# Kernel optimization log

Hardware: AMD Instinct MI355X
Metric: run time of the kernel (lower is better)

Reference implementation:

```python
import jax, jax.numpy as jnp
import numpy as np

# dims chosen per input_specs / init_kwargs
B, S, D_IN, UNITS, WIN = 4, 2048, 512, 64, 32
W = 2 * WIN + 1  # max window length


def setup_inputs() -> dict:
    key = jax.random.key(0)
    ks = jax.random.split(key, 8)
    p = lambda k, shape: jax.random.normal(k, shape, dtype=jnp.float32) * 0.02
    return {
        "query": jax.random.normal(ks[0], (B, S, D_IN), dtype=jnp.float32),
        "value": jax.random.normal(ks[1], (B, S, D_IN), dtype=jnp.float32),
        "Wq": p(ks[2], (D_IN, UNITS)), "bq": jnp.zeros((UNITS,), jnp.float32),
        "Wk": p(ks[3], (D_IN, UNITS)), "bk": jnp.zeros((UNITS,), jnp.float32),
        "Wv": p(ks[4], (D_IN, UNITS)), "bv": jnp.zeros((UNITS,), jnp.float32),
    }


def reference(query, value, Wq, bq, Wk, bk, Wv, bv):
    # Dense projections (query stream -> Q, value stream -> K and V)
    Q = query @ Wq + bq
    K = value @ Wk + bk
    V = value @ Wv + bv

    i = np.arange(S)
    start = np.maximum(i - WIN, 0)            # [S]
    end = np.minimum(i + WIN + 1, S)          # [S]
    lengths = end - start                      # [S] window length per position
    offsets = np.concatenate([[0], np.cumsum(lengths)[:-1]])
    L = int(lengths.sum())                     # total output seq length (concat of all windows)

    idx = start[:, None] + np.arange(W)[None, :]   # [S, W] window token indices
    valid = idx < end[:, None]                      # [S, W] which slots exist
    idx_c = np.minimum(idx, S - 1)                  # clamp for safe gather

    idx_c = jnp.asarray(idx_c)
    valid_j = jnp.asarray(valid)

    # Gather overlapping windows: [B, S, W, UNITS]
    Ql = Q[:, idx_c]
    Kl = K[:, idx_c]
    Vl = V[:, idx_c]

    # Faithful to original: ALL window rows act as queries for window i.
    scale = 1.0 / jnp.sqrt(jnp.asarray(UNITS, dtype=Q.dtype))
    scores = jnp.einsum("bswd,bsud->bswu", Ql, Kl) * scale  # [B, S, W, W]
    neg = jnp.finfo(scores.dtype).min
    scores = jnp.where(valid_j[None, :, None, :], scores, neg)  # mask padded keys
    weights = jax.nn.softmax(scores, axis=-1)
    out_local = jnp.einsum("bswu,bsud->bswd", weights, Vl)  # [B, S, W, UNITS]

    # Concat valid rows of every window along seq axis -> [B, L, UNITS]
    flat_pos = jnp.asarray(offsets)[:, None] + jnp.arange(W)[None, :]  # [S, W]
    flat_pos = jnp.where(valid_j, flat_pos, L)  # invalid rows dumped in slot L
    out = jnp.zeros((Q.shape[0], L + 1, UNITS), dtype=out_local.dtype)
    out = out.at[:, flat_pos.reshape(-1)].set(out_local.reshape(Q.shape[0], -1, UNITS))
    return out[:, :L]
```

## Files before the change

kernel.cpp:

```cpp
#include <hip/hip_runtime.h>
#include <hip/hip_bf16.h>

#define BB 4
#define SS 2048
#define DIN 512
#define UU 64
#define WINR 32
#define LTOT 132064
#define GQ 16
#define VST 200

typedef __attribute__((ext_vector_type(8))) short short8;
typedef __attribute__((ext_vector_type(4))) float float4v;
typedef __attribute__((ext_vector_type(4))) uint uint4v;

static __device__ __forceinline__ ushort f2bf(float f) {
    union { __hip_bfloat16 h; ushort u; } c;
    c.h = __float2bfloat16(f);
    return c.u;
}
static __device__ __forceinline__ float bf2f(ushort u) {
    union { float f; uint v; } c;
    c.v = ((uint)u) << 16;
    return c.f;
}
static __device__ __forceinline__ float bfbits(uint u) {
    union { float f; uint v; } c;
    c.v = u;
    return c.f;
}

__device__ __forceinline__ int offs_of(int s) {
    int a = s < (SS - 33) ? s : (SS - 33);
    int m = (s - 33) > 0 ? (s - 33) : 0;
    return a * (a - 1) / 2 + 33 * a + (s - a) * SS - m * (m + 1) / 2;
}

__global__ __launch_bounds__(256) void prep_w(
    const float* __restrict__ Wq, const float* __restrict__ Wk, const float* __restrict__ Wv,
    ushort* __restrict__ Wt)
{
    __shared__ float T[64][65];
    const int mtx = blockIdx.x >> 3;
    const int kc  = blockIdx.x & 7;
    const float* W = (mtx == 0) ? Wq : ((mtx == 1) ? Wk : Wv);
    const int tid = threadIdx.x;
    for (int idx = tid; idx < 64 * 64; idx += 256) {
        const int k = idx >> 6, n = idx & 63;
        T[n][k] = W[(size_t)(kc * 64 + k) * UU + n];
    }
    __syncthreads();
    for (int idx = tid; idx < 64 * 64; idx += 256) {
        const int n = idx >> 6, kl = idx & 63;
        Wt[(size_t)mtx * UU * DIN + (size_t)n * DIN + kc * 64 + kl] = f2bf(T[n][kl]);
    }
}

__global__ __launch_bounds__(256) void qkv_mfma(
    const float* __restrict__ query, const float* __restrict__ value,
    const ushort* __restrict__ Wt,
    const float* __restrict__ bq, const float* __restrict__ bk, const float* __restrict__ bv,
    float* __restrict__ Qs, ushort* __restrict__ Kf, ushort* __restrict__ Vf)
{
    __shared__ float red[4][16 * UU];
    const int bid = blockIdx.x;
    const int mtx = bid >> 9;
    const int rt  = bid & 511;
    const int tid = threadIdx.x;
    const int kq = tid >> 6;
    const int lane = tid & 63;
    const int m16 = lane & 15, quad = lane >> 4;

    const float* X = (mtx == 0) ? query : value;
    const float* Xrow = X + (size_t)(rt * 16 + m16) * DIN + kq * 128 + quad * 8;
    const ushort* Wm = Wt + (size_t)mtx * UU * DIN + (size_t)m16 * DIN + kq * 128 + quad * 8;

    float4v acc[4];
#pragma unroll
    for (int nb = 0; nb < 4; ++nb) acc[nb] = (float4v){0.f, 0.f, 0.f, 0.f};

#pragma unroll
    for (int kk = 0; kk < 4; ++kk) {
        const float4 xa = *(const float4*)(Xrow + kk * 32);
        const float4 xb = *(const float4*)(Xrow + kk * 32 + 4);
        short8 a;
        a[0] = (short)f2bf(xa.x); a[1] = (short)f2bf(xa.y);
        a[2] = (short)f2bf(xa.z); a[3] = (short)f2bf(xa.w);
        a[4] = (short)f2bf(xb.x); a[5] = (short)f2bf(xb.y);
        a[6] = (short)f2bf(xb.z); a[7] = (short)f2bf(xb.w);
#pragma unroll
        for (int nb = 0; nb < 4; ++nb) {
            const short8 bfr = *(const short8*)(Wm + (size_t)nb * 16 * DIN + kk * 32);
            acc[nb] = __builtin_amdgcn_mfma_f32_16x16x32_bf16(a, bfr, acc[nb], 0, 0, 0);
        }
    }

#pragma unroll
    for (int nb = 0; nb < 4; ++nb)
#pragma unroll
        for (int reg = 0; reg < 4; ++reg)
            red[kq][(quad * 4 + reg) * UU + nb * 16 + m16] = acc[nb][reg];
    __syncthreads();

    const float* bias = (mtx == 0) ? bq : ((mtx == 1) ? bk : bv);
#pragma unroll
    for (int i = 0; i < 4; ++i) {
        const int e = tid + 256 * i;
        const int col = e & 63, row = e >> 6;
        float s = red[0][e] + red[1][e] + red[2][e] + red[3][e] + bias[col];
        const size_t gi = (size_t)(rt * 16 + row) * UU + col;
        if (mtx == 0)      Qs[gi] = s * 0.125f;
        else if (mtx == 1) Kf[gi] = f2bf(s);
        else               Vf[gi] = f2bf(s);
    }
}

__global__ __launch_bounds__(1024, 8) void attn_kernel(
    const float* __restrict__ Qs, const ushort* __restrict__ Kf,
    const ushort* __restrict__ Vf, float* __restrict__ out)
{
    __shared__ __align__(16) ushort Vt[UU * VST];
    __shared__ __align__(16) float  evf[GQ * VST];

    const int blk = blockIdx.x;
    const int b = blk >> 7;
    const int q0 = (blk & 127) << 4;
    const int tid = threadIdx.x;
    const int lane = tid & 63;
    const int wq = __builtin_amdgcn_readfirstlane(tid >> 6);

    const int j0 = max(q0 - 2 * WINR, 0);
    const int j1 = min(q0 + GQ - 1 + 2 * WINR + 1, SS);
    const int nw = j1 - j0;

    {
        const uint4v z = (uint4v){0u, 0u, 0u, 0u};
        uint4v* V4 = (uint4v*)Vt;
        uint4v* E4 = (uint4v*)evf;
        for (int i = tid; i < 1600; i += 1024) V4[i] = z;
        for (int i = tid; i < 800;  i += 1024) E4[i] = z;
    }
    __syncthreads();

    if (wq >= 9) {
        const uint* Vg = (const uint*)(Vf + ((size_t)b * SS + j0) * UU);
        for (int idx = tid - 9 * 64; idx < nw * 32; idx += 7 * 64) {
            const int j = idx >> 5, d2 = idx & 31;
            const uint v = Vg[idx];
            Vt[(2 * d2) * VST + 40 + j]     = (ushort)v;
            Vt[(2 * d2 + 1) * VST + 40 + j] = (ushort)(v >> 16);
        }
    } else {
        const int t = wq;
        const int m16 = lane & 15, quad = lane >> 4;
        const int jb = j0 + 16 * t + m16;
        const int jr = jb < SS ? jb : SS - 1;
        const ushort* kr = Kf + ((size_t)b * SS + jr) * UU + quad * 8;
        const float*  qr = Qs + ((size_t)b * SS + q0 + m16) * UU + quad * 8;
        const short8 kb0 = *(const short8*)(kr);
        const short8 kb1 = *(const short8*)(kr + 32);
        short8 ah0, al0, ah1, al1;
#pragma unroll
        for (int e = 0; e < 8; ++e) {
            const float qa = qr[e], qb = qr[e + 32];
            const ushort h0 = f2bf(qa);
            ah0[e] = (short)h0; al0[e] = (short)f2bf(qa - bf2f(h0));
            const ushort h1 = f2bf(qb);
            ah1[e] = (short)h1; al1[e] = (short)f2bf(qb - bf2f(h1));
        }
        float4v acc = (float4v){0.f, 0.f, 0.f, 0.f};
        acc = __builtin_amdgcn_mfma_f32_16x16x32_bf16(ah0, kb0, acc, 0, 0, 0);
        acc = __builtin_amdgcn_mfma_f32_16x16x32_bf16(al0, kb0, acc, 0, 0, 0);
        acc = __builtin_amdgcn_mfma_f32_16x16x32_bf16(ah1, kb1, acc, 0, 0, 0);
        acc = __builtin_amdgcn_mfma_f32_16x16x32_bf16(al1, kb1, acc, 0, 0, 0);
#pragma unroll
        for (int r = 0; r < 4; ++r) {
            const int m = quad * 4 + r;
            const int d = jb - (q0 + m);
            const bool in = (d >= -64) && (d <= 64) && (jb < SS);
            evf[m * VST + 40 + 16 * t + m16] = in ? __expf(acc[r]) : 0.f;
        }
    }
    __syncthreads();

    const int qi = q0 + wq;
    const int s_lo = max(qi - WINR, 0);
    const int s_hi = min(qi + WINR, SS - 1);
    const int a = (s_lo - j0 - 7) & 7;
    const int s_start = s_lo - a;
    const int I_s = s_start - j0 + 8;
    const int I_f = I_s - 7;
    const int A0 = I_f + 72;

    const ushort* vrow = Vt + lane * VST;
    const float*  erow = evf + wq * VST;

    float accA = 0.f, denA = 0.f, accR = 0.f, denR = 0.f;
#pragma unroll
    for (int t = 0; t < 9; ++t) {
        const int base = I_f + 8 * t;
        const uint4v  vv = *(const uint4v*)(vrow + base);
        const float4v e0 = *(const float4v*)(erow + base);
        const float4v e1 = *(const float4v*)(erow + base + 4);
#pragma unroll
        for (int k = 0; k < 8; ++k) {
            const float e = (k < 4) ? e0[k] : e1[k - 4];
            const uint wv = vv[k >> 1];
            const float v = (k & 1) ? bfbits(wv & 0xffff0000u) : bfbits(wv << 16);
            accA = fmaf(e, v, accA);
            denA += e;
        }
    }

    float pE7 = erow[I_s];
    float pV7 = bf2f(vrow[I_s]);

    int off = offs_of(s_lo);
    float* outb = out + (size_t)b * LTOT * UU;
    const int ng = (s_hi - s_start + 8) >> 3;
    for (int g = 0; g < ng; ++g) {
        const int Ab = A0 + 8 * g;
        const uint4v  Av  = *(const uint4v*)(vrow + Ab);
        const float4v Ae0 = *(const float4v*)(erow + Ab);
        const float4v Ae1 = *(const float4v*)(erow + Ab + 4);
        const int Rb = I_f + 8 * (g + 1);
        const uint4v  Rv  = *(const uint4v*)(vrow + Rb);
        const float4v Re0 = *(const float4v*)(erow + Rb);
        const float4v Re1 = *(const float4v*)(erow + Rb + 4);
        int s = s_start + 8 * g;
#pragma unroll
        for (int k = 0; k < 8; ++k, ++s) {
            if (s >= s_lo && s <= s_hi) {
                const int st = (s - WINR > 0) ? s - WINR : 0;
                const int en = (s + WINR + 1 < SS) ? s + WINR + 1 : SS;
                const float r = __builtin_amdgcn_rcpf(denA - denR);
                outb[(size_t)(off + qi - st) * UU + lane] = (accA - accR) * r;
                off += en - st;
            }
            {
                const float e = (k < 4) ? Ae0[k] : Ae1[k - 4];
                const uint wv = Av[k >> 1];
                const float v = (k & 1) ? bfbits(wv & 0xffff0000u) : bfbits(wv << 16);
                accA = fmaf(e, v, accA);
                denA += e;
            }
            {
                float e, v;
                if (k == 0) { e = pE7; v = pV7; }
                else {
                    const int m = k - 1;
                    e = (m < 4) ? Re0[m] : Re1[m - 4];
                    const uint wv = Rv[m >> 1];
                    v = (m & 1) ? bfbits(wv & 0xffff0000u) : bfbits(wv << 16);
                }
                accR = fmaf(e, v, accR);
                denR += e;
            }
        }
        pE7 = Re1[3];
        pV7 = bfbits(Rv[3] & 0xffff0000u);
    }
}

extern "C" void kernel_launch(void* const* d_in, const int* in_sizes, int n_in,
                              void* d_out, int out_size, void* d_ws, size_t ws_size,
                              hipStream_t stream) {
    const float* query = (const float*)d_in[0];
    const float* value = (const float*)d_in[1];
    const float* Wq = (const float*)d_in[2];
    const float* bq = (const float*)d_in[3];
    const float* Wk = (const float*)d_in[4];
    const float* bk = (const float*)d_in[5];
    const float* Wv = (const float*)d_in[6];
    const float* bv = (const float*)d_in[7];
    float* out = (float*)d_out;

    float* Qs = (float*)d_ws;
    ushort* Kf = (ushort*)(Qs + (size_t)BB * SS * UU);
    ushort* Vf = Kf + (size_t)BB * SS * UU;
    ushort* Wt = (ushort*)((float*)d_out + (size_t)out_size) - (size_t)3 * UU * DIN;

    prep_w<<<24, 256, 0, stream>>>(Wq, Wk, Wv, Wt);
    qkv_mfma<<<3 * 512, 256, 0, stream>>>(query, value, Wt, bq, bk, bv, Qs, Kf, Vf);
    attn_kernel<<<512, 1024, 0, stream>>>(Qs, Kf, Vf, out);
}
```

Before: 198.6 us.

## Fuse K/V projections, store V transposed, add fast interior output path

The projection kernel now computes K and V in the same block, so each value tile is read and converted to bf16 once instead of twice. This cuts the grid from 1536 to 1024 blocks. V is written to global memory in a transposed [b][d][j] layout, which lets the attention kernel fill its shared V tile with 16-byte vector copies instead of scattered 16-bit stores. Interior query groups get a simplified output loop with a fixed stride and no per-position window bookkeeping. The trade-offs are a padded reduction buffer, uncoalesced 2-byte transposed V writes, and a duplicated code path for edge groups.

Result: no change. 198.6 us (-0.0%).

```diff
diff --git a/kernel.cpp b/kernel.cpp
--- a/kernel.cpp
+++ b/kernel.cpp
@@ -9,6 +9,7 @@
 #define LTOT 132064
 #define GQ 16
 #define VST 200
+#define RST 65
 
 typedef __attribute__((ext_vector_type(8))) short short8;
 typedef __attribute__((ext_vector_type(4))) float float4v;
@@ -60,24 +61,28 @@
     const float* __restrict__ query, const float* __restrict__ value,
     const ushort* __restrict__ Wt,
     const float* __restrict__ bq, const float* __restrict__ bk, const float* __restrict__ bv,
-    float* __restrict__ Qs, ushort* __restrict__ Kf, ushort* __restrict__ Vf)
+    float* __restrict__ Qs, ushort* __restrict__ Kf, ushort* __restrict__ Vtg)
 {
-    __shared__ float red[4][16 * UU];
+    __shared__ float red[4][16 * RST];
     const int bid = blockIdx.x;
-    const int mtx = bid >> 9;
-    const int rt  = bid & 511;
+    const bool isQ = bid < 512;
+    const int rt  = isQ ? bid : bid - 512;
     const int tid = threadIdx.x;
     const int kq = tid >> 6;
     const int lane = tid & 63;
     const int m16 = lane & 15, quad = lane >> 4;
 
-    const float* X = (mtx == 0) ? query : value;
+    const float* X = isQ ? query : value;
     const float* Xrow = X + (size_t)(rt * 16 + m16) * DIN + kq * 128 + quad * 8;
-    const ushort* Wm = Wt + (size_t)mtx * UU * DIN + (size_t)m16 * DIN + kq * 128 + quad * 8;
-
-    float4v acc[4];
-#pragma unroll
-    for (int nb = 0; nb < 4; ++nb) acc[nb] = (float4v){0.f, 0.f, 0.f, 0.f};
+    const ushort* Wm = Wt + (size_t)(isQ ? 0 : 1) * UU * DIN
+                          + (size_t)m16 * DIN + kq * 128 + quad * 8;
+
+    float4v acc0[4], acc1[4];
+#pragma unroll
+    for (int nb = 0; nb < 4; ++nb) {
+        acc0[nb] = (float4v){0.f, 0.f, 0.f, 0.f};
+        acc1[nb] = (float4v){0.f, 0.f, 0.f, 0.f};
+    }
 
 #pragma unroll
     for (int kk = 0; kk < 4; ++kk) {
@@ -90,8 +95,15 @@
         a[6] = (short)f2bf(xb.z); a[7] = (short)f2bf(xb.w);
 #pragma unroll
         for (int nb = 0; nb < 4; ++nb) {
-            const short8 bfr = *(const short8*)(Wm + (size_t)nb * 16 * DIN + kk * 32);
-            acc[nb] = __builtin_amdgcn_mfma_f32_16x16x32_bf16(a, bfr, acc[nb], 0, 0, 0);
+            const short8 b0 = *(const short8*)(Wm + (size_t)nb * 16 * DIN + kk * 32);
+            acc0[nb] = __builtin_amdgcn_mfma_f32_16x16x32_bf16(a, b0, acc0[nb], 0, 0, 0);
+        }
+        if (!isQ) {
+#pragma unroll
+            for (int nb = 0; nb < 4; ++nb) {
+                const short8 b1 = *(const short8*)(Wm + (size_t)UU * DIN + (size_t)nb * 16 * DIN + kk * 32);
+                acc1[nb] = __builtin_amdgcn_mfma_f32_16x16x32_bf16(a, b1, acc1[nb], 0, 0, 0);
+            }
         }
     }
 
@@ -99,25 +111,44 @@
     for (int nb = 0; nb < 4; ++nb)
 #pragma unroll
         for (int reg = 0; reg < 4; ++reg)
-            red[kq][(quad * 4 + reg) * UU + nb * 16 + m16] = acc[nb][reg];
-    __syncthreads();
-
-    const float* bias = (mtx == 0) ? bq : ((mtx == 1) ? bk : bv);
+            red[kq][(quad * 4 + reg) * RST + nb * 16 + m16] = acc0[nb][reg];
+    __syncthreads();
+
+    const float* bias0 = isQ ? bq : bk;
 #pragma unroll
     for (int i = 0; i < 4; ++i) {
         const int e = tid + 256 * i;
         const int col = e & 63, row = e >> 6;
-        float s = red[0][e] + red[1][e] + red[2][e] + red[3][e] + bias[col];
+        const int ra = row * RST + col;
+        float s = red[0][ra] + red[1][ra] + red[2][ra] + red[3][ra] + bias0[col];
         const size_t gi = (size_t)(rt * 16 + row) * UU + col;
-        if (mtx == 0)      Qs[gi] = s * 0.125f;
-        else if (mtx == 1) Kf[gi] = f2bf(s);
-        else               Vf[gi] = f2bf(s);
+        if (isQ) Qs[gi] = s * 0.125f;
+        else     Kf[gi] = f2bf(s);
+    }
+    if (isQ) return;
+
+    __syncthreads();
+#pragma unroll
+    for (int nb = 0; nb < 4; ++nb)
+#pragma unroll
+        for (int reg = 0; reg < 4; ++reg)
+            red[kq][(quad * 4 + reg) * RST + nb * 16 + m16] = acc1[nb][reg];
+    __syncthreads();
+#pragma unroll
+    for (int i = 0; i < 4; ++i) {
+        const int e = tid + 256 * i;
+        const int row = e & 15, col = e >> 4;
+        const int ra = row * RST + col;
+        const float s = red[0][ra] + red[1][ra] + red[2][ra] + red[3][ra] + bv[col];
+        const int r = rt * 16 + row;
+        const int bb = r >> 11, j = r & 2047;
+        Vtg[(((size_t)(bb * UU + col)) << 11) + j] = f2bf(s);
     }
 }
 
 __global__ __launch_bounds__(1024, 8) void attn_kernel(
     const float* __restrict__ Qs, const ushort* __restrict__ Kf,
-    const ushort* __restrict__ Vf, float* __restrict__ out)
+    const ushort* __restrict__ Vtg, float* __restrict__ out)
 {
     __shared__ __align__(16) ushort Vt[UU * VST];
     __shared__ __align__(16) float  evf[GQ * VST];
@@ -143,12 +174,13 @@
     __syncthreads();
 
     if (wq >= 9) {
-        const uint* Vg = (const uint*)(Vf + ((size_t)b * SS + j0) * UU);
-        for (int idx = tid - 9 * 64; idx < nw * 32; idx += 7 * 64) {
-            const int j = idx >> 5, d2 = idx & 31;
-            const uint v = Vg[idx];
-            Vt[(2 * d2) * VST + 40 + j]     = (ushort)v;
-            Vt[(2 * d2 + 1) * VST + 40 + j] = (ushort)(v >> 16);
+        const ushort* Vsrc = Vtg + ((size_t)b << 17);
+        for (int idx = tid - 9 * 64; idx < UU * 18; idx += 7 * 64) {
+            const int d = idx / 18, t = idx - d * 18;
+            if (t * 8 < nw) {
+                const uint4v v = *(const uint4v*)(Vsrc + ((size_t)d << 11) + j0 + t * 8);
+                *(uint4v*)(Vt + d * VST + 40 + t * 8) = v;
+            }
         }
     } else {
         const int t = wq;
@@ -215,50 +247,95 @@
     float pE7 = erow[I_s];
     float pV7 = bf2f(vrow[I_s]);
 
-    int off = offs_of(s_lo);
     float* outb = out + (size_t)b * LTOT * UU;
-    const int ng = (s_hi - s_start + 8) >> 3;
-    for (int g = 0; g < ng; ++g) {
-        const int Ab = A0 + 8 * g;
-        const uint4v  Av  = *(const uint4v*)(vrow + Ab);
-        const float4v Ae0 = *(const float4v*)(erow + Ab);
-        const float4v Ae1 = *(const float4v*)(erow + Ab + 4);
-        const int Rb = I_f + 8 * (g + 1);
-        const uint4v  Rv  = *(const uint4v*)(vrow + Rb);
-        const float4v Re0 = *(const float4v*)(erow + Rb);
-        const float4v Re1 = *(const float4v*)(erow + Rb + 4);
-        int s = s_start + 8 * g;
-#pragma unroll
-        for (int k = 0; k < 8; ++k, ++s) {
-            if (s >= s_lo && s <= s_hi) {
-                const int st = (s - WINR > 0) ? s - WINR : 0;
-                const int en = (s + WINR + 1 < SS) ? s + WINR + 1 : SS;
-                const float r = __builtin_amdgcn_rcpf(denA - denR);
-                outb[(size_t)(off + qi - st) * UU + lane] = (accA - accR) * r;
-                off += en - st;
+
+    if (q0 >= 64 && q0 <= SS - 80) {
+        float* pst = outb + ((size_t)offs_of(s_lo) + 64) * UU + lane;
+        for (int g = 0; g < 9; ++g) {
+            const int Ab = A0 + 8 * g;
+            const uint4v  Av  = *(const uint4v*)(vrow + Ab);
+            const float4v Ae0 = *(const float4v*)(erow + Ab);
+            const float4v Ae1 = *(const float4v*)(erow + Ab + 4);
+            const int Rb = I_f + 8 * (g + 1);
+            const uint4v  Rv  = *(const uint4v*)(vrow + Rb);
+            const float4v Re0 = *(const float4v*)(erow + Rb);
+            const float4v Re1 = *(const float4v*)(erow + Rb + 4);
+#pragma unroll
+            for (int k = 0; k < 8; ++k) {
+                const bool real = (g == 0) ? (k >= a) : ((g < 8) ? true : (k <= a));
+                if (real) {
+                    const float r = __builtin_amdgcn_rcpf(denA - denR);
+                    *pst = (accA - accR) * r;
+                    pst += (size_t)64 * UU;
+                }
+                {
+                    const float e = (k < 4) ? Ae0[k] : Ae1[k - 4];
+                    const uint wv = Av[k >> 1];
+                    const float v = (k & 1) ? bfbits(wv & 0xffff0000u) : bfbits(wv << 16);
+                    accA = fmaf(e, v, accA);
+                    denA += e;
+                }
+                {
+                    float e, v;
+                    if (k == 0) { e = pE7; v = pV7; }
+                    else {
+                        const int m = k - 1;
+                        e = (m < 4) ? Re0[m] : Re1[m - 4];
+                        const uint wv = Rv[m >> 1];
+                        v = (m & 1) ? bfbits(wv & 0xffff0000u) : bfbits(wv << 16);
+                    }
+                    accR = fmaf(e, v, accR);
+                    denR += e;
+                }
             }
-            {
-                const float e = (k < 4) ? Ae0[k] : Ae1[k - 4];
-                const uint wv = Av[k >> 1];
-                const float v = (k & 1) ? bfbits(wv & 0xffff0000u) : bfbits(wv << 16);
-                accA = fmaf(e, v, accA);
-                denA += e;
+            pE7 = Re1[3];
+            pV7 = bfbits(Rv[3] & 0xffff0000u);
+        }
+    } else {
+        int off = offs_of(s_lo);
+        const int ng = (s_hi - s_start + 8) >> 3;
+        for (int g = 0; g < ng; ++g) {
+            const int Ab = A0 + 8 * g;
+            const uint4v  Av  = *(const uint4v*)(vrow + Ab);
+            const float4v Ae0 = *(const float4v*)(erow + Ab);
+            const float4v Ae1 = *(const float4v*)(erow + Ab + 4);
+            const int Rb = I_f + 8 * (g + 1);
+            const uint4v  Rv  = *(const uint4v*)(vrow + Rb);
+            const float4v Re0 = *(const float4v*)(erow + Rb);
+            const float4v Re1 = *(const float4v*)(erow + Rb + 4);
+            int s = s_start + 8 * g;
+#pragma unroll
+            for (int k = 0; k < 8; ++k, ++s) {
+                if (s >= s_lo && s <= s_hi) {
+                    const int st = (s - WINR > 0) ? s - WINR : 0;
+                    const int en = (s + WINR + 1 < SS) ? s + WINR + 1 : SS;
+                    const float r = __builtin_amdgcn_rcpf(denA - denR);
+                    outb[(size_t)(off + qi - st) * UU + lane] = (accA - accR) * r;
+                    off += en - st;
+                }
+                {
+                    const float e = (k < 4) ? Ae0[k] : Ae1[k - 4];
+                    const uint wv = Av[k >> 1];
+                    const float v = (k & 1) ? bfbits(wv & 0xffff0000u) : bfbits(wv << 16);
+                    accA = fmaf(e, v, accA);
+                    denA += e;
+                }
+                {
+                    float e, v;
+                    if (k == 0) { e = pE7; v = pV7; }
+                    else {
+                        const int m = k - 1;
+                        e = (m < 4) ? Re0[m] : Re1[m - 4];
+                        const uint wv = Rv[m >> 1];
+                        v = (m & 1) ? bfbits(wv & 0xffff0000u) : bfbits(wv << 16);
+                    }
+                    accR = fmaf(e, v, accR);
+                    denR += e;
+                }
             }
-            {
-                float e, v;
-                if (k == 0) { e = pE7; v = pV7; }
-                else {
-                    const int m = k - 1;
-                    e = (m < 4) ? Re0[m] : Re1[m - 4];
-                    const uint wv = Rv[m >> 1];
-                    v = (m & 1) ? bfbits(wv & 0xffff0000u) : bfbits(wv << 16);
-                }
-                accR = fmaf(e, v, accR);
-                denR += e;
-            }
-        }
-        pE7 = Re1[3];
-        pV7 = bfbits(Rv[3] & 0xffff0000u);
+            pE7 = Re1[3];
+            pV7 = bfbits(Rv[3] & 0xffff0000u);
+        }
     }
 }
 
@@ -277,10 +354,10 @@
 
     float* Qs = (float*)d_ws;
     ushort* Kf = (ushort*)(Qs + (size_t)BB * SS * UU);
-    ushort* Vf = Kf + (size_t)BB * SS * UU;
+    ushort* Vtg = Kf + (size_t)BB * SS * UU;
     ushort* Wt = (ushort*)((float*)d_out + (size_t)out_size) - (size_t)3 * UU * DIN;
 
     prep_w<<<24, 256, 0, stream>>>(Wq, Wk, Wv, Wt);
-    qkv_mfma<<<3 * 512, 256, 0, stream>>>(query, value, Wt, bq, bk, bv, Qs, Kf, Vf);
-    attn_kernel<<<512, 1024, 0, stream>>>(Qs, Kf, Vf, out);
-}
+    qkv_mfma<<<1024, 256, 0, stream>>>(query, value, Wt, bq, bk, bv, Qs, Kf, Vtg);
+    attn_kernel<<<512, 1024, 0, stream>>>(Qs, Kf, Vtg, out);
+}
```
